# Kernel tuning notes

Measured on AMD Instinct MI355X. Metric: run time of the kernel, lower is better.

Reference implementation:

```python
import jax, jax.numpy as jnp
import numpy as np

B, C, H, W = 8, 256, 64, 64
NUM_HEADS = 4


def setup_inputs() -> dict:
    key = jax.random.key(0)
    ks = jax.random.split(key, 6)
    s = 0.02  # small init scale for 1x1 conv weights
    return {
        "x": jax.random.normal(ks[0], (B, C, H, W), jnp.float32),
        "cproj": jax.random.normal(ks[1], (B, C, H, W), jnp.float32),
        "wq": jax.random.normal(ks[2], (C, C), jnp.float32) * s,
        "bq": jnp.zeros((C,), jnp.float32),
        "wkv": jax.random.normal(ks[3], (2 * C, C), jnp.float32) * s,
        "bkv": jnp.zeros((2 * C,), jnp.float32),
        "wo": jax.random.normal(ks[4], (C, C), jnp.float32) * s,  # zero_module in torch; random here for a meaningful baseline
        "bo": jnp.zeros((C,), jnp.float32),
    }


def reference(x, cproj, wq, bq, wkv, bkv, wo, bo):
    Bb, Cc, Hh, Ww = x.shape
    N = Hh * Ww
    h = NUM_HEADS
    d = Cc // h
    scale = 1.0 / jnp.sqrt(jnp.sqrt(jnp.asarray(Cc, jnp.float32)))

    xf = x.reshape(Bb, Cc, N)
    cf = cproj.reshape(Bb, Cc, N)

    # 1x1 convs == channel matmuls
    Q = jnp.einsum('oc,bcn->bon', wq, xf) + bq[None, :, None]           # (B,C,N)
    KV = jnp.einsum('oc,bcn->bon', wkv, cf) + bkv[None, :, None]        # (B,2C,N)
    K, V = KV[:, :Cc], KV[:, Cc:]

    # softmax over channel-dim-within-head for q, over spatial N for k
    q = jax.nn.softmax(Q.reshape(Bb, h, d, N) * scale, axis=2).reshape(Bb, Cc, N)
    k = jax.nn.softmax(K.reshape(Bb, h, d, N), axis=3).reshape(Bb, Cc, N)

    # linear-attention: (B,C,C) context, then project back to N — note heads are mixed, per original bmm
    context = jnp.einsum('bcn,bdn->bcd', k, V)
    out = jnp.einsum('bcd,bdn->bcn', context, q)

    out = jnp.einsum('oc,bcn->bon', wo, out) + bo[None, :, None]
    return out.reshape(Bb, Cc, Hh, Ww)
```

## Files before the change

### kernel.cpp

```cpp
#include <hip/hip_runtime.h>

#define B_ 8
#define C_ 256
#define N_ 4096
#define NSPLIT 8

typedef float f32x4 __attribute__((ext_vector_type(4)));
typedef __bf16 bf16x8 __attribute__((ext_vector_type(8)));
typedef unsigned short u16x8 __attribute__((ext_vector_type(8)));
typedef unsigned short u16x4 __attribute__((ext_vector_type(4)));

__device__ __forceinline__ unsigned short f2bf(float f) {
  unsigned u = __float_as_uint(f);
  u += 0x7fff + ((u >> 16) & 1);
  return (unsigned short)(u >> 16);
}

__device__ __forceinline__ f32x4 mfma16(bf16x8 a, bf16x8 b, f32x4 c) {
  return __builtin_amdgcn_mfma_f32_16x16x32_bf16(a, b, c, 0, 0, 0);
}

typedef __attribute__((address_space(1))) const void* gvp;
typedef __attribute__((address_space(3))) void* lvp;
__device__ __forceinline__ void gld16(const void* g, void* l) {
  __builtin_amdgcn_global_load_lds((gvp)g, (lvp)l, 16, 0, 0);
}

template <int ROWS>
__device__ __forceinline__ void stage(unsigned short* lds, const unsigned short* g,
                                      int ld, int w, int lane) {
  const int r8 = lane >> 3;
  const int ce = ((lane & 7) ^ r8) << 3;
  const unsigned short* gp = g + (size_t)(w * (ROWS / 4) + r8) * ld + ce;
  unsigned short* lp = lds + w * (ROWS / 4) * 64;
#pragma unroll
  for (int i = 0; i < ROWS / 32; i++)
    gld16(gp + (size_t)(i * 8) * ld, lp + i * 512);
}

__device__ __forceinline__ bf16x8 frag(const unsigned short* lds, int row, int kc) {
  return *(const bf16x8*)(lds + row * 64 + ((kc ^ (row & 7)) << 3));
}

__global__ __launch_bounds__(256) void castw(
    const float* __restrict__ wq, const float* __restrict__ wkv,
    const float* __restrict__ wo, unsigned short* __restrict__ wqb,
    unsigned short* __restrict__ wkvb, unsigned short* __restrict__ wob) {
  int i = (blockIdx.x * 256 + threadIdx.x) * 4;
  const float* src;
  unsigned short* dst;
  int off;
  if (i < 65536) { src = wq; dst = wqb; off = i; }
  else if (i < 196608) { src = wkv; dst = wkvb; off = i - 65536; }
  else { src = wo; dst = wob; off = i - 196608; }
  float4 v = *(const float4*)(src + off);
  *(u16x4*)(dst + off) = (u16x4){f2bf(v.x), f2bf(v.y), f2bf(v.z), f2bf(v.w)};
}

__global__ __launch_bounds__(256) void transpose_cast(
    const float* __restrict__ x, const float* __restrict__ cp,
    unsigned short* __restrict__ xT, unsigned short* __restrict__ cpT) {
  __shared__ unsigned short tr[64][72];
  const int z = blockIdx.z, b = z >> 1;
  const float* src = (z & 1) ? cp : x;
  unsigned short* dst = (z & 1) ? cpT : xT;
  const int c0 = blockIdx.y * 64, n0 = blockIdx.x * 64;
  const int t = threadIdx.x;
  const int r0 = (t >> 4) * 4;
  const int nq = (t & 15) * 4;
  const float* sp = src + ((size_t)b * C_ + c0 + r0) * N_ + n0 + nq;
  float4 v[4];
#pragma unroll
  for (int i = 0; i < 4; i++) v[i] = *(const float4*)(sp + (size_t)i * N_);
#pragma unroll
  for (int j = 0; j < 4; j++) {
    u16x4 o = (u16x4){f2bf(((const float*)&v[0])[j]), f2bf(((const float*)&v[1])[j]),
                      f2bf(((const float*)&v[2])[j]), f2bf(((const float*)&v[3])[j])};
    *(u16x4*)&tr[nq + j][r0] = o;
  }
  __syncthreads();
  const int nr = t >> 2, cg = (t & 3) * 16;
  unsigned short* dp = dst + ((size_t)b * N_ + n0 + nr) * C_ + c0 + cg;
  *(u16x8*)dp = *(const u16x8*)&tr[nr][cg];
  *(u16x8*)(dp + 8) = *(const u16x8*)&tr[nr][cg + 8];
}

__global__ __launch_bounds__(256) void qproj(
    const unsigned short* __restrict__ wqb, const unsigned short* __restrict__ xT,
    const float* __restrict__ bq, unsigned short* __restrict__ qT) {
  __shared__ __align__(16) unsigned short As[256 * 64];
  __shared__ __align__(16) unsigned short Bs[64 * 64];
  const int b = blockIdx.z, n0 = blockIdx.x * 64;
  const int tid = threadIdx.x, lane = tid & 63, w = tid >> 6;
  const int m0w = w * 64;
  const int colL = lane & 15, kq = lane >> 4, quad = lane >> 4;
  const unsigned short* Bg = xT + ((size_t)b * N_ + n0) * C_;

  f32x4 acc[4][4];
#pragma unroll
  for (int i = 0; i < 4; i++)
#pragma unroll
    for (int j = 0; j < 4; j++) acc[i][j] = (f32x4){0.f, 0.f, 0.f, 0.f};

  for (int kt = 0; kt < 4; kt++) {
    stage<256>(As, wqb + kt * 64, C_, w, lane);
    stage<64>(Bs, Bg + kt * 64, C_, w, lane);
    __syncthreads();
#pragma unroll
    for (int ks = 0; ks < 2; ks++) {
      bf16x8 af[4], bf[4];
#pragma unroll
      for (int mt = 0; mt < 4; mt++) af[mt] = frag(As, m0w + mt * 16 + colL, ks * 4 + kq);
#pragma unroll
      for (int nt = 0; nt < 4; nt++) bf[nt] = frag(Bs, nt * 16 + colL, ks * 4 + kq);
#pragma unroll
      for (int mt = 0; mt < 4; mt++)
#pragma unroll
        for (int nt = 0; nt < 4; nt++) acc[mt][nt] = mfma16(af[mt], bf[nt], acc[mt][nt]);
    }
    __syncthreads();
  }

#pragma unroll
  for (int nt = 0; nt < 4; nt++) {
    float v[16];
    float mx = -1e30f;
#pragma unroll
    for (int mt = 0; mt < 4; mt++)
#pragma unroll
      for (int r = 0; r < 4; r++) {
        int m = m0w + mt * 16 + quad * 4 + r;
        float val = (acc[mt][nt][r] + bq[m]) * 0.25f;
        v[mt * 4 + r] = val;
        mx = fmaxf(mx, val);
      }
    mx = fmaxf(mx, __shfl_xor(mx, 16));
    mx = fmaxf(mx, __shfl_xor(mx, 32));
    float s = 0.f;
#pragma unroll
    for (int j = 0; j < 16; j++) { v[j] = __expf(v[j] - mx); s += v[j]; }
    s += __shfl_xor(s, 16);
    s += __shfl_xor(s, 32);
    float inv = 1.0f / s;
    const int n = n0 + nt * 16 + colL;
    unsigned short* qb = qT + ((size_t)b * N_ + n) * C_ + m0w;
#pragma unroll
    for (int mt = 0; mt < 4; mt++) {
      u16x4 o = (u16x4){f2bf(v[mt * 4 + 0] * inv), f2bf(v[mt * 4 + 1] * inv),
                        f2bf(v[mt * 4 + 2] * inv), f2bf(v[mt * 4 + 3] * inv)};
      *(u16x4*)(qb + mt * 16 + quad * 4) = o;
    }
  }
}

__global__ __launch_bounds__(256) void kvproj(
    const unsigned short* __restrict__ wkvb, const unsigned short* __restrict__ cpT,
    const float* __restrict__ bkv, float* __restrict__ Kf,
    unsigned short* __restrict__ Vb) {
  __shared__ __align__(16) unsigned short As[512 * 64];
  __shared__ __align__(16) unsigned short Bs[64 * 64];
  const int b = blockIdx.z, n0 = blockIdx.x * 64;
  const int tid = threadIdx.x, lane = tid & 63, w = tid >> 6;
  const int m0w = w * 128;
  const int colL = lane & 15, kq = lane >> 4, quad = lane >> 4;
  const unsigned short* Bg = cpT + ((size_t)b * N_ + n0) * C_;

  f32x4 acc[8][4];
#pragma unroll
  for (int i = 0; i < 8; i++)
#pragma unroll
    for (int j = 0; j < 4; j++) acc[i][j] = (f32x4){0.f, 0.f, 0.f, 0.f};

  for (int kt = 0; kt < 4; kt++) {
    stage<512>(As, wkvb + kt * 64, C_, w, lane);
    stage<64>(Bs, Bg + kt * 64, C_, w, lane);
    __syncthreads();
#pragma unroll
    for (int ks = 0; ks < 2; ks++) {
      bf16x8 bf[4];
#pragma unroll
      for (int nt = 0; nt < 4; nt++) bf[nt] = frag(Bs, nt * 16 + colL, ks * 4 + kq);
#pragma unroll
      for (int mt = 0; mt < 8; mt++) {
        bf16x8 af = frag(As, m0w + mt * 16 + colL, ks * 4 + kq);
#pragma unroll
        for (int nt = 0; nt < 4; nt++) acc[mt][nt] = mfma16(af, bf[nt], acc[mt][nt]);
      }
    }
    __syncthreads();
  }

#pragma unroll
  for (int mt = 0; mt < 8; mt++)
#pragma unroll
    for (int r = 0; r < 4; r++) {
      int m = m0w + mt * 16 + quad * 4 + r;
      float bias = bkv[m];
      if (m < C_) {
        float* kr = Kf + ((size_t)b * C_ + m) * N_ + n0;
#pragma unroll
        for (int nt = 0; nt < 4; nt++) kr[nt * 16 + colL] = acc[mt][nt][r] + bias;
      } else {
        unsigned short* vr = Vb + ((size_t)b * C_ + m - C_) * N_ + n0;
#pragma unroll
        for (int nt = 0; nt < 4; nt++) vr[nt * 16 + colL] = f2bf(acc[mt][nt][r] + bias);
      }
    }
}

__global__ __launch_bounds__(256) void ksoftmax(const float* __restrict__ Kf,
                                                unsigned short* __restrict__ kb) {
  const int b = blockIdx.x >> 8, c = blockIdx.x & 255;
  const float* row = Kf + ((size_t)b * C_ + c) * N_;
  unsigned short* orow = kb + ((size_t)b * C_ + c) * N_;
  const int t = threadIdx.x, lane = t & 63, wv = t >> 6;
  __shared__ float red[8];

  float4 v[4];
  float mx = -1e30f;
#pragma unroll
  for (int i = 0; i < 4; i++) {
    v[i] = *(const float4*)&row[i * 1024 + t * 4];
    mx = fmaxf(fmaxf(fmaxf(mx, v[i].x), fmaxf(v[i].y, v[i].z)), v[i].w);
  }
#pragma unroll
  for (int o = 32; o > 0; o >>= 1) mx = fmaxf(mx, __shfl_down(mx, o));
  if (lane == 0) red[wv] = mx;
  __syncthreads();
  mx = fmaxf(fmaxf(red[0], red[1]), fmaxf(red[2], red[3]));

  float s = 0.f;
#pragma unroll
  for (int i = 0; i < 4; i++) {
    v[i].x = __expf(v[i].x - mx); v[i].y = __expf(v[i].y - mx);
    v[i].z = __expf(v[i].z - mx); v[i].w = __expf(v[i].w - mx);
    s += v[i].x + v[i].y + v[i].z + v[i].w;
  }
#pragma unroll
  for (int o = 32; o > 0; o >>= 1) s += __shfl_down(s, o);
  if (lane == 0) red[4 + wv] = s;
  __syncthreads();
  float inv = 1.0f / (red[4] + red[5] + red[6] + red[7]);
#pragma unroll
  for (int i = 0; i < 4; i++) {
    u16x4 o = (u16x4){f2bf(v[i].x * inv), f2bf(v[i].y * inv),
                      f2bf(v[i].z * inv), f2bf(v[i].w * inv)};
    *(u16x4*)&orow[i * 1024 + t * 4] = o;
  }
}

__global__ __launch_bounds__(256) void ctx_part(
    const unsigned short* __restrict__ kb, const unsigned short* __restrict__ Vb,
    float* __restrict__ ctxp) {
  __shared__ __align__(16) unsigned short As[128 * 64];
  __shared__ __align__(16) unsigned short Bs[64 * 64];
  const int z = blockIdx.z, b = z >> 3, s = z & 7;
  const int m0 = blockIdx.y * 128, n0 = blockIdx.x * 64;
  const int tid = threadIdx.x, lane = tid & 63, w = tid >> 6;
  const int m0w = (w & 1) * 64, n0w = (w >> 1) * 32;
  const int colL = lane & 15, kq = lane >> 4, quad = lane >> 4;
  const unsigned short* Ag = kb + ((size_t)b * C_ + m0) * N_;
  const unsigned short* Bg = Vb + ((size_t)b * C_ + n0) * N_;
  const int kbeg = s * (N_ / NSPLIT);

  f32x4 acc[4][2];
#pragma unroll
  for (int i = 0; i < 4; i++)
#pragma unroll
    for (int j = 0; j < 2; j++) acc[i][j] = (f32x4){0.f, 0.f, 0.f, 0.f};

  for (int kt = 0; kt < (N_ / NSPLIT) / 64; kt++) {
    stage<128>(As, Ag + kbeg + kt * 64, N_, w, lane);
    stage<64>(Bs, Bg + kbeg + kt * 64, N_, w, lane);
    __syncthreads();
#pragma unroll
    for (int ks = 0; ks < 2; ks++) {
      bf16x8 af[4], bf[2];
#pragma unroll
      for (int mt = 0; mt < 4; mt++) af[mt] = frag(As, m0w + mt * 16 + colL, ks * 4 + kq);
#pragma unroll
      for (int nt = 0; nt < 2; nt++) bf[nt] = frag(Bs, n0w + nt * 16 + colL, ks * 4 + kq);
#pragma unroll
      for (int mt = 0; mt < 4; mt++)
#pragma unroll
        for (int nt = 0; nt < 2; nt++) acc[mt][nt] = mfma16(af[mt], bf[nt], acc[mt][nt]);
    }
    __syncthreads();
  }

  float* outp = ctxp + ((size_t)s * B_ + b) * C_ * C_;
#pragma unroll
  for (int mt = 0; mt < 4; mt++)
#pragma unroll
    for (int nt = 0; nt < 2; nt++)
#pragma unroll
      for (int r = 0; r < 4; r++) {
        int m = m0 + m0w + mt * 16 + quad * 4 + r;
        int n = n0 + n0w + nt * 16 + colL;
        outp[(size_t)m * C_ + n] = acc[mt][nt][r];
      }
}

__global__ __launch_bounds__(256) void ctx_reduce_t(const float* __restrict__ ctxp,
                                                    unsigned short* __restrict__ ctxsT) {
  __shared__ unsigned short t[64][72];
  const int b = blockIdx.z, c0 = blockIdx.y * 64, d0 = blockIdx.x * 64;
  const int tid = threadIdx.x;
  const int cl = tid >> 2, dg = (tid & 3) * 16;
  const float* base = ctxp + ((size_t)b * C_ + c0 + cl) * C_ + d0 + dg;
  float acc[16];
#pragma unroll
  for (int j = 0; j < 16; j++) acc[j] = 0.f;
  for (int s = 0; s < NSPLIT; s++) {
    const float* p = base + (size_t)s * B_ * C_ * C_;
#pragma unroll
    for (int j = 0; j < 16; j += 4) {
      float4 v = *(const float4*)(p + j);
      acc[j] += v.x; acc[j + 1] += v.y; acc[j + 2] += v.z; acc[j + 3] += v.w;
    }
  }
#pragma unroll
  for (int j = 0; j < 16; j++) t[dg + j][cl] = f2bf(acc[j]);
  __syncthreads();
  const int dr = tid >> 2, cg = (tid & 3) * 16;
  unsigned short* dp = ctxsT + ((size_t)b * C_ + d0 + dr) * C_ + c0 + cg;
  *(u16x8*)dp = *(const u16x8*)&t[dr][cg];
  *(u16x8*)(dp + 8) = *(const u16x8*)&t[dr][cg + 8];
}

__global__ __launch_bounds__(256) void oproj(
    const unsigned short* __restrict__ wob, const unsigned short* __restrict__ ctxsT,
    unsigned short* __restrict__ ctx2) {
  __shared__ __align__(16) unsigned short As[128 * 64];
  __shared__ __align__(16) unsigned short Bs[128 * 64];
  const int b = blockIdx.z, m0 = blockIdx.y * 128, n0 = blockIdx.x * 128;
  const int tid = threadIdx.x, lane = tid & 63, w = tid >> 6;
  const int m0w = (w >> 1) * 64, n0w = (w & 1) * 64;
  const int colL = lane & 15, kq = lane >> 4, quad = lane >> 4;
  const unsigned short* Ag = wob + (size_t)m0 * C_;
  const unsigned short* Bg = ctxsT + ((size_t)b * C_ + n0) * C_;

  f32x4 acc[4][4];
#pragma unroll
  for (int i = 0; i < 4; i++)
#pragma unroll
    for (int j = 0; j < 4; j++) acc[i][j] = (f32x4){0.f, 0.f, 0.f, 0.f};

  for (int kt = 0; kt < 4; kt++) {
    stage<128>(As, Ag + kt * 64, C_, w, lane);
    stage<128>(Bs, Bg + kt * 64, C_, w, lane);
    __syncthreads();
#pragma unroll
    for (int ks = 0; ks < 2; ks++) {
      bf16x8 af[4], bf[4];
#pragma unroll
      for (int mt = 0; mt < 4; mt++) af[mt] = frag(As, m0w + mt * 16 + colL, ks * 4 + kq);
#pragma unroll
      for (int nt = 0; nt < 4; nt++) bf[nt] = frag(Bs, n0w + nt * 16 + colL, ks * 4 + kq);
#pragma unroll
      for (int mt = 0; mt < 4; mt++)
#pragma unroll
        for (int nt = 0; nt < 4; nt++) acc[mt][nt] = mfma16(af[mt], bf[nt], acc[mt][nt]);
    }
    __syncthreads();
  }

  unsigned short* ob = ctx2 + (size_t)b * C_ * C_;
#pragma unroll
  for (int mt = 0; mt < 4; mt++)
#pragma unroll
    for (int nt = 0; nt < 4; nt++)
#pragma unroll
      for (int r = 0; r < 4; r++) {
        int m = m0 + m0w + mt * 16 + quad * 4 + r;
        int n = n0 + n0w + nt * 16 + colL;
        ob[(size_t)m * C_ + n] = f2bf(acc[mt][nt][r]);
      }
}

__global__ __launch_bounds__(256) void outgemm(
    const unsigned short* __restrict__ ctx2, const unsigned short* __restrict__ qT,
    const float* __restrict__ bo, float* __restrict__ out) {
  __shared__ __align__(16) unsigned short As[256 * 64];
  __shared__ __align__(16) unsigned short Bs[64 * 64];
  const int b = blockIdx.z, n0 = blockIdx.x * 64;
  const int tid = threadIdx.x, lane = tid & 63, w = tid >> 6;
  const int m0w = w * 64;
  const int colL = lane & 15, kq = lane >> 4, quad = lane >> 4;
  const unsigned short* Ag = ctx2 + (size_t)b * C_ * C_;
  const unsigned short* Bg = qT + ((size_t)b * N_ + n0) * C_;

  f32x4 acc[4][4];
#pragma unroll
  for (int i = 0; i < 4; i++)
#pragma unroll
    for (int j = 0; j < 4; j++) acc[i][j] = (f32x4){0.f, 0.f, 0.f, 0.f};

  for (int kt = 0; kt < 4; kt++) {
    stage<256>(As, Ag + kt * 64, C_, w, lane);
    stage<64>(Bs, Bg + kt * 64, C_, w, lane);
    __syncthreads();
#pragma unroll
    for (int ks = 0; ks < 2; ks++) {
      bf16x8 af[4], bf[4];
#pragma unroll
      for (int mt = 0; mt < 4; mt++) af[mt] = frag(As, m0w + mt * 16 + colL, ks * 4 + kq);
#pragma unroll
      for (int nt = 0; nt < 4; nt++) bf[nt] = frag(Bs, nt * 16 + colL, ks * 4 + kq);
#pragma unroll
      for (int mt = 0; mt < 4; mt++)
#pragma unroll
        for (int nt = 0; nt < 4; nt++) acc[mt][nt] = mfma16(af[mt], bf[nt], acc[mt][nt]);
    }
    __syncthreads();
  }

  float* ob = out + (size_t)b * C_ * N_;
#pragma unroll
  for (int mt = 0; mt < 4; mt++)
#pragma unroll
    for (int r = 0; r < 4; r++) {
      int m = m0w + mt * 16 + quad * 4 + r;
      float bias = bo[m];
#pragma unroll
      for (int nt = 0; nt < 4; nt++) {
        int n = n0 + nt * 16 + colL;
        ob[(size_t)m * N_ + n] = acc[mt][nt][r] + bias;
      }
    }
}

extern "C" void kernel_launch(void* const* d_in, const int* in_sizes, int n_in,
                              void* d_out, int out_size, void* d_ws, size_t ws_size,
                              hipStream_t stream) {
  const float* x     = (const float*)d_in[0];
  const float* cproj = (const float*)d_in[1];
  const float* wq    = (const float*)d_in[2];
  const float* bq    = (const float*)d_in[3];
  const float* wkv   = (const float*)d_in[4];
  const float* bkv   = (const float*)d_in[5];
  const float* wo    = (const float*)d_in[6];
  const float* bo    = (const float*)d_in[7];
  float* out = (float*)d_out;

  unsigned short* xT    = (unsigned short*)d_ws;
  unsigned short* cpT   = xT + 8388608;
  unsigned short* qT    = cpT + 8388608;
  float*          Kf    = (float*)(qT + 8388608);
  unsigned short* Vb    = (unsigned short*)(Kf + 8388608);
  unsigned short* wqb   = Vb + 8388608;
  unsigned short* wkvb  = wqb + 65536;
  unsigned short* wob   = wkvb + 131072;
  unsigned short* ctxsT = wob + 65536;
  unsigned short* ctx2  = ctxsT + 524288;
  unsigned short* kb    = xT;
  float*          ctxp  = (float*)cpT;

  castw<<<256, 256, 0, stream>>>(wq, wkv, wo, wqb, wkvb, wob);
  transpose_cast<<<dim3(64, 4, 16), 256, 0, stream>>>(x, cproj, xT, cpT);
  qproj<<<dim3(64, 1, 8), 256, 0, stream>>>(wqb, xT, bq, qT);
  kvproj<<<dim3(64, 1, 8), 256, 0, stream>>>(wkvb, cpT, bkv, Kf, Vb);
  ksoftmax<<<2048, 256, 0, stream>>>(Kf, kb);
  ctx_part<<<dim3(4, 2, 64), 256, 0, stream>>>(kb, Vb, ctxp);
  ctx_reduce_t<<<dim3(4, 4, 8), 256, 0, stream>>>(ctxp, ctxsT);
  oproj<<<dim3(2, 2, 8), 256, 0, stream>>>(wob, ctxsT, ctx2);
  outgemm<<<dim3(64, 1, 8), 256, 0, stream>>>(ctx2, qT, bo, out);
}
```

Before: 213.5 us.

## Fuse input transpose-cast into projection GEMMs with register-prefetched fp32 loads

Removes the separate transpose_cast kernel. The q and kv projection GEMMs now read the fp32 x and cproj directly, convert them to bf16 and transpose them into a padded LDS tile. The next K-tile is prefetched into registers while MFMAs run. This avoids writing and re-reading two bf16 transposed copies of the inputs, at the cost of more global traffic per GEMM (fp32 reads) and scalar-ish LDS writes. The workspace layout is reorganized so that kb and ctxp no longer alias the removed buffers.

After: 199.3 us. -6.6%, faster.

```diff
diff --git a/kernel.cpp b/kernel.cpp
--- a/kernel.cpp
+++ b/kernel.cpp
@@ -40,6 +40,32 @@
 
 __device__ __forceinline__ bf16x8 frag(const unsigned short* lds, int row, int kc) {
   return *(const bf16x8*)(lds + row * 64 + ((kc ^ (row & 7)) << 3));
+}
+
+__device__ __forceinline__ void loadB(float4* pbv, const float* src, int ld,
+                                      int n0, int kt, int w, int lane) {
+  const int nf = lane & 15, kg = lane >> 4;
+  const float* sp = src + (size_t)(kt * 64 + w * 16 + kg * 4) * ld + n0 + 4 * nf;
+#pragma unroll
+  for (int i = 0; i < 4; i++) pbv[i] = *(const float4*)(sp + (size_t)i * ld);
+}
+__device__ __forceinline__ void writeB(unsigned short* Bs, const float4* pbv,
+                                       int w, int lane) {
+  const int nf = lane & 15, kg = lane >> 4;
+  const int k0 = w * 16 + kg * 4;
+#pragma unroll
+  for (int j = 0; j < 4; j++) {
+    u16x4 o = (u16x4){f2bf(((const float*)&pbv[0])[j]), f2bf(((const float*)&pbv[1])[j]),
+                      f2bf(((const float*)&pbv[2])[j]), f2bf(((const float*)&pbv[3])[j])};
+    *(u16x4*)&Bs[(4 * nf + j) * 68 + k0] = o;
+  }
+}
+__device__ __forceinline__ bf16x8 fragB(const unsigned short* Bs, int n, int k8) {
+  union { u16x4 q[2]; bf16x8 b; } u;
+  const unsigned short* p = Bs + n * 68 + k8 * 8;
+  u.q[0] = *(const u16x4*)p;
+  u.q[1] = *(const u16x4*)(p + 4);
+  return u.b;
 }
 
 __global__ __launch_bounds__(256) void castw(
@@ -57,44 +83,16 @@
   *(u16x4*)(dst + off) = (u16x4){f2bf(v.x), f2bf(v.y), f2bf(v.z), f2bf(v.w)};
 }
 
-__global__ __launch_bounds__(256) void transpose_cast(
-    const float* __restrict__ x, const float* __restrict__ cp,
-    unsigned short* __restrict__ xT, unsigned short* __restrict__ cpT) {
-  __shared__ unsigned short tr[64][72];
-  const int z = blockIdx.z, b = z >> 1;
-  const float* src = (z & 1) ? cp : x;
-  unsigned short* dst = (z & 1) ? cpT : xT;
-  const int c0 = blockIdx.y * 64, n0 = blockIdx.x * 64;
-  const int t = threadIdx.x;
-  const int r0 = (t >> 4) * 4;
-  const int nq = (t & 15) * 4;
-  const float* sp = src + ((size_t)b * C_ + c0 + r0) * N_ + n0 + nq;
-  float4 v[4];
-#pragma unroll
-  for (int i = 0; i < 4; i++) v[i] = *(const float4*)(sp + (size_t)i * N_);
-#pragma unroll
-  for (int j = 0; j < 4; j++) {
-    u16x4 o = (u16x4){f2bf(((const float*)&v[0])[j]), f2bf(((const float*)&v[1])[j]),
-                      f2bf(((const float*)&v[2])[j]), f2bf(((const float*)&v[3])[j])};
-    *(u16x4*)&tr[nq + j][r0] = o;
-  }
-  __syncthreads();
-  const int nr = t >> 2, cg = (t & 3) * 16;
-  unsigned short* dp = dst + ((size_t)b * N_ + n0 + nr) * C_ + c0 + cg;
-  *(u16x8*)dp = *(const u16x8*)&tr[nr][cg];
-  *(u16x8*)(dp + 8) = *(const u16x8*)&tr[nr][cg + 8];
-}
-
 __global__ __launch_bounds__(256) void qproj(
-    const unsigned short* __restrict__ wqb, const unsigned short* __restrict__ xT,
+    const unsigned short* __restrict__ wqb, const float* __restrict__ x,
     const float* __restrict__ bq, unsigned short* __restrict__ qT) {
   __shared__ __align__(16) unsigned short As[256 * 64];
-  __shared__ __align__(16) unsigned short Bs[64 * 64];
+  __shared__ __align__(16) unsigned short Bs[64 * 68];
   const int b = blockIdx.z, n0 = blockIdx.x * 64;
   const int tid = threadIdx.x, lane = tid & 63, w = tid >> 6;
   const int m0w = w * 64;
   const int colL = lane & 15, kq = lane >> 4, quad = lane >> 4;
-  const unsigned short* Bg = xT + ((size_t)b * N_ + n0) * C_;
+  const float* xb = x + (size_t)b * C_ * N_;
 
   f32x4 acc[4][4];
 #pragma unroll
@@ -102,17 +100,21 @@
 #pragma unroll
     for (int j = 0; j < 4; j++) acc[i][j] = (f32x4){0.f, 0.f, 0.f, 0.f};
 
+  float4 pbv[4];
+  loadB(pbv, xb, N_, n0, 0, w, lane);
+
   for (int kt = 0; kt < 4; kt++) {
+    writeB(Bs, pbv, w, lane);
     stage<256>(As, wqb + kt * 64, C_, w, lane);
-    stage<64>(Bs, Bg + kt * 64, C_, w, lane);
-    __syncthreads();
+    __syncthreads();
+    if (kt < 3) loadB(pbv, xb, N_, n0, kt + 1, w, lane);
 #pragma unroll
     for (int ks = 0; ks < 2; ks++) {
       bf16x8 af[4], bf[4];
 #pragma unroll
       for (int mt = 0; mt < 4; mt++) af[mt] = frag(As, m0w + mt * 16 + colL, ks * 4 + kq);
 #pragma unroll
-      for (int nt = 0; nt < 4; nt++) bf[nt] = frag(Bs, nt * 16 + colL, ks * 4 + kq);
+      for (int nt = 0; nt < 4; nt++) bf[nt] = fragB(Bs, nt * 16 + colL, ks * 4 + kq);
 #pragma unroll
       for (int mt = 0; mt < 4; mt++)
 #pragma unroll
@@ -154,16 +156,16 @@
 }
 
 __global__ __launch_bounds__(256) void kvproj(
-    const unsigned short* __restrict__ wkvb, const unsigned short* __restrict__ cpT,
+    const unsigned short* __restrict__ wkvb, const float* __restrict__ cp,
     const float* __restrict__ bkv, float* __restrict__ Kf,
     unsigned short* __restrict__ Vb) {
   __shared__ __align__(16) unsigned short As[512 * 64];
-  __shared__ __align__(16) unsigned short Bs[64 * 64];
+  __shared__ __align__(16) unsigned short Bs[64 * 68];
   const int b = blockIdx.z, n0 = blockIdx.x * 64;
   const int tid = threadIdx.x, lane = tid & 63, w = tid >> 6;
   const int m0w = w * 128;
   const int colL = lane & 15, kq = lane >> 4, quad = lane >> 4;
-  const unsigned short* Bg = cpT + ((size_t)b * N_ + n0) * C_;
+  const float* cpb = cp + (size_t)b * C_ * N_;
 
   f32x4 acc[8][4];
 #pragma unroll
@@ -171,15 +173,19 @@
 #pragma unroll
     for (int j = 0; j < 4; j++) acc[i][j] = (f32x4){0.f, 0.f, 0.f, 0.f};
 
+  float4 pbv[4];
+  loadB(pbv, cpb, N_, n0, 0, w, lane);
+
   for (int kt = 0; kt < 4; kt++) {
+    writeB(Bs, pbv, w, lane);
     stage<512>(As, wkvb + kt * 64, C_, w, lane);
-    stage<64>(Bs, Bg + kt * 64, C_, w, lane);
-    __syncthreads();
+    __syncthreads();
+    if (kt < 3) loadB(pbv, cpb, N_, n0, kt + 1, w, lane);
 #pragma unroll
     for (int ks = 0; ks < 2; ks++) {
       bf16x8 bf[4];
 #pragma unroll
-      for (int nt = 0; nt < 4; nt++) bf[nt] = frag(Bs, nt * 16 + colL, ks * 4 + kq);
+      for (int nt = 0; nt < 4; nt++) bf[nt] = fragB(Bs, nt * 16 + colL, ks * 4 + kq);
 #pragma unroll
       for (int mt = 0; mt < 8; mt++) {
         bf16x8 af = frag(As, m0w + mt * 16 + colL, ks * 4 + kq);
@@ -443,23 +449,20 @@
   const float* bo    = (const float*)d_in[7];
   float* out = (float*)d_out;
 
-  unsigned short* xT    = (unsigned short*)d_ws;
-  unsigned short* cpT   = xT + 8388608;
-  unsigned short* qT    = cpT + 8388608;
+  unsigned short* qT    = (unsigned short*)d_ws;
   float*          Kf    = (float*)(qT + 8388608);
   unsigned short* Vb    = (unsigned short*)(Kf + 8388608);
-  unsigned short* wqb   = Vb + 8388608;
+  unsigned short* kb    = Vb + 8388608;
+  float*          ctxp  = (float*)(kb + 8388608);
+  unsigned short* wqb   = (unsigned short*)(ctxp + 4194304);
   unsigned short* wkvb  = wqb + 65536;
   unsigned short* wob   = wkvb + 131072;
   unsigned short* ctxsT = wob + 65536;
   unsigned short* ctx2  = ctxsT + 524288;
-  unsigned short* kb    = xT;
-  float*          ctxp  = (float*)cpT;
 
   castw<<<256, 256, 0, stream>>>(wq, wkv, wo, wqb, wkvb, wob);
-  transpose_cast<<<dim3(64, 4, 16), 256, 0, stream>>>(x, cproj, xT, cpT);
-  qproj<<<dim3(64, 1, 8), 256, 0, stream>>>(wqb, xT, bq, qT);
-  kvproj<<<dim3(64, 1, 8), 256, 0, stream>>>(wkvb, cpT, bkv, Kf, Vb);
+  qproj<<<dim3(64, 1, 8), 256, 0, stream>>>(wqb, x, bq, qT);
+  kvproj<<<dim3(64, 1, 8), 256, 0, stream>>>(wkvb, cproj, bkv, Kf, Vb);
   ksoftmax<<<2048, 256, 0, stream>>>(Kf, kb);
   ctx_part<<<dim3(4, 2, 64), 256, 0, stream>>>(kb, Vb, ctxp);
   ctx_reduce_t<<<dim3(4, 4, 8), 256, 0, stream>>>(ctxp, ctxsT);
```
